# Performance work log

Measured on AMD Instinct MI355X. Metric: run time of the kernel, lower is better.

The kernel has to match this reference:

```python
import jax, jax.numpy as jnp
import numpy as np

B, C, L = 8, 1024, 4096
CTX = 768
NUM_GROUPS = 8
EPS = 1e-5
HEAD_DIM = C  # num_heads = 1 (only shape-consistent config of the module)


def setup_inputs() -> dict:
    key = jax.random.key(0)
    ks = jax.random.split(key, 8)
    s = 0.02
    return {
        "x": jax.random.normal(ks[0], (B, C, L), jnp.float32),
        "context": jax.random.normal(ks[1], (B, CTX), jnp.float32),
        "gn_gamma": jnp.ones((C,), jnp.float32),
        "gn_beta": jnp.zeros((C,), jnp.float32),
        "ln_gamma": jnp.ones((CTX,), jnp.float32),
        "ln_beta": jnp.zeros((CTX,), jnp.float32),
        "Wq": jax.random.normal(ks[2], (C, C), jnp.float32) * s,
        "bq": jnp.zeros((C,), jnp.float32),
        "Wkv": jax.random.normal(ks[3], (2 * C, CTX), jnp.float32) * s,
        "bkv": jnp.zeros((2 * C,), jnp.float32),
        "Wp": jax.random.normal(ks[4], (C, C), jnp.float32) * s,
        "bp": jnp.zeros((C,), jnp.float32),
    }


def group_norm(x, gamma, beta):
    # x: (B, C, L) -> normalize within each of NUM_GROUPS groups over (C//G, L)
    b, c, l = x.shape
    xg = x.reshape(b, NUM_GROUPS, c // NUM_GROUPS, l)
    mu = xg.mean(axis=(2, 3), keepdims=True)
    var = xg.var(axis=(2, 3), keepdims=True)
    xg = (xg - mu) * jax.lax.rsqrt(var + EPS)
    return xg.reshape(b, c, l) * gamma[None, :, None] + beta[None, :, None]


def layer_norm(x, gamma, beta):
    mu = x.mean(axis=-1, keepdims=True)
    var = x.var(axis=-1, keepdims=True)
    return (x - mu) * jax.lax.rsqrt(var + EPS) * gamma + beta


def reference(x, context, gn_gamma, gn_beta, ln_gamma, ln_beta,
              Wq, bq, Wkv, bkv, Wp, bp):
    residual = x
    xn = group_norm(x, gn_gamma, gn_beta)                   # (B, C, L)
    ctx = layer_norm(context, ln_gamma, ln_beta)            # (B, CTX)
    # 1x1 conv Q projection == channel GEMM
    q = jnp.einsum('bcl,oc->bol', xn, Wq) + bq[None, :, None]  # (B, C, L)
    kv = ctx @ Wkv.T + bkv                                  # (B, 2C)
    k, v = kv[:, :C], kv[:, C:]                             # each (B, C) = (B, head_dim)
    scale = HEAD_DIM ** (-0.5)
    # per-position score against the single context key; softmax over L
    attn = jax.nn.softmax(jnp.einsum('bcl,bc->bl', q, k) * scale, axis=-1)  # (B, L)
    # broadcast-weighted outer product (fused form of expand+mul+sum over heads=1)
    out = attn[:, None, :] * v[:, :, None]                  # (B, C, L)
    out = jnp.einsum('bcl,oc->bol', out, Wp) + bp[None, :, None]
    return residual + out
```

## Files before the change

### kernel.cpp

```cpp
#include <hip/hip_runtime.h>
#include <math.h>

#define NB   8
#define NC   1024
#define NL   4096
#define NCTX 768
#define EPSV 1e-5f
#define SCALEV 0.03125f

typedef float floatx4 __attribute__((ext_vector_type(4)));

enum : int {
  OFF_KV    = 0,
  OFF_PV    = 16384,
  OFF_QP    = 24576,
  OFF_SPART = 548864,
  OFF_TPART = 552960,
  OFF_ATTN  = 1077248,
  OFF_S     = 1110016,
  WS_FLOATS = 1110024
};

__device__ __forceinline__ float breduce_sum(float v, float* red) {
  int t = threadIdx.x;
  red[t] = v; __syncthreads();
  for (int s = 128; s > 0; s >>= 1) { if (t < s) red[t] += red[t + s]; __syncthreads(); }
  float r = red[0]; __syncthreads();
  return r;
}
__device__ __forceinline__ float wave_sum(float v) {
  #pragma unroll
  for (int off = 32; off > 0; off >>= 1) v += __shfl_xor(v, off, 64);
  return v;
}

__global__ void k_head(const float* __restrict__ ctx, const float* __restrict__ lng,
                       const float* __restrict__ lnb, const float* __restrict__ Wkv,
                       const float* __restrict__ bkv, const float* __restrict__ Wq,
                       const float* __restrict__ Wp,  float* __restrict__ ws) {
  __shared__ __align__(16) float scf[8 * NCTX];
  __shared__ float sk[8 * 16];
  int t = threadIdx.x, bid = blockIdx.x;
  int wave = t >> 6, lane = t & 63;
  if (bid == 0 && t < NB) ws[OFF_S + t] = 0.f;

  if (bid < 128) {
    #pragma unroll
    for (int bb = 0; bb < 2; bb++) {
      int b = wave * 2 + bb;
      const float* row = ctx + b * NCTX;
      float v[12];
      float s = 0.f;
      #pragma unroll
      for (int k = 0; k < 12; k++) { v[k] = row[lane + 64 * k]; s += v[k]; }
      float mu = wave_sum(s) * (1.0f / NCTX);
      float s2 = 0.f;
      #pragma unroll
      for (int k = 0; k < 12; k++) { float d = v[k] - mu; s2 = fmaf(d, d, s2); }
      float rstd = rsqrtf(wave_sum(s2) * (1.0f / NCTX) + EPSV);
      #pragma unroll
      for (int k = 0; k < 12; k++) {
        int j = lane + 64 * k;
        scf[b * NCTX + j] = (v[k] - mu) * rstd * lng[j] + lnb[j];
      }
    }
    __syncthreads();
    const float4* W4 = reinterpret_cast<const float4*>(Wkv);
    const float4* sc4 = reinterpret_cast<const float4*>(scf);
    #pragma unroll
    for (int rr = 0; rr < 4; rr++) {
      int j = bid * 16 + wave * 4 + rr;
      float4 wv0 = W4[(size_t)j * 192 + lane];
      float4 wv1 = W4[(size_t)j * 192 + lane + 64];
      float4 wv2 = W4[(size_t)j * 192 + lane + 128];
      #pragma unroll
      for (int b = 0; b < 8; b++) {
        const float4* sb = sc4 + b * 192;
        float4 c0 = sb[lane], c1 = sb[lane + 64], c2 = sb[lane + 128];
        float a = wv0.x*c0.x + wv0.y*c0.y + wv0.z*c0.z + wv0.w*c0.w
                + wv1.x*c1.x + wv1.y*c1.y + wv1.z*c1.z + wv1.w*c1.w
                + wv2.x*c2.x + wv2.y*c2.y + wv2.z*c2.z + wv2.w*c2.w;
        a = wave_sum(a);
        if (lane == 0) {
          ws[OFF_KV + b * 2048 + j] = a + bkv[j];
          if (bid < 64) sk[b * 16 + (wave * 4 + rr)] = a + bkv[j];
        }
      }
    }
    if (bid < 64) {
      __syncthreads();
      const float4* Wq4 = reinterpret_cast<const float4*>(Wq);
      float4 acc[8];
      #pragma unroll
      for (int b = 0; b < 8; b++) acc[b] = make_float4(0.f, 0.f, 0.f, 0.f);
      int o0 = bid * 16;
      #pragma unroll 4
      for (int oi = 0; oi < 16; oi++) {
        float4 w = Wq4[(size_t)(o0 + oi) * 256 + t];
        #pragma unroll
        for (int b = 0; b < 8; b++) {
          float kk = sk[b * 16 + oi];
          acc[b].x = fmaf(kk, w.x, acc[b].x);
          acc[b].y = fmaf(kk, w.y, acc[b].y);
          acc[b].z = fmaf(kk, w.z, acc[b].z);
          acc[b].w = fmaf(kk, w.w, acc[b].w);
        }
      }
      float4* qp4 = reinterpret_cast<float4*>(ws + OFF_QP);
      #pragma unroll
      for (int b = 0; b < 8; b++) qp4[(bid * 8 + b) * 256 + t] = acc[b];
    }
  } else {
    const float4* Wp4 = reinterpret_cast<const float4*>(Wp);
    int pid = bid - 128;
    float acc = 0.f;
    for (int idx = pid * 256 + t; idx < 262144; idx += 128 * 256) {
      float4 v = Wp4[idx];
      acc += v.x + v.y + v.z + v.w;
    }
    asm volatile("" :: "v"(acc));
  }
}

__global__ void k_pass1(const float* __restrict__ x, const float* __restrict__ gng,
                        float* __restrict__ ws) {
  __shared__ float red[256];
  __shared__ float sw[64];
  __shared__ __align__(16) float4 part[192];
  int t  = threadIdx.x;
  int lc = blockIdx.x;
  int cs = blockIdx.y;
  int bz = blockIdx.z;
  int b = bz >> 3, g = bz & 7;
  int c0 = g * 128 + cs * 64;
  {
    int cl = t & 63, sp = t >> 6;
    const float* qp = ws + OFF_QP + b * 1024 + c0 + cl;
    float s = 0.f;
    #pragma unroll 4
    for (int oc = sp * 16; oc < sp * 16 + 16; oc++) s += qp[(size_t)oc * 8192];
    red[t] = s;
    __syncthreads();
    if (t < 64) sw[t] = gng[c0 + t] * ((red[t] + red[t + 64]) + (red[t + 128] + red[t + 192]));
    __syncthreads();
  }
  int tl = t & 63, q = t >> 6;
  int l4 = lc * 64 + tl;
  const float4* x4 = reinterpret_cast<const float4*>(x);
  float4 tacc = make_float4(0.f, 0.f, 0.f, 0.f);
  float s1 = 0.f, s2 = 0.f;
  #pragma unroll 4
  for (int ci = q * 16; ci < q * 16 + 16; ci++) {
    float w = sw[ci];
    float4 v = x4[(size_t)(b * NC + c0 + ci) * 1024 + l4];
    tacc.x = fmaf(w, v.x, tacc.x);
    tacc.y = fmaf(w, v.y, tacc.y);
    tacc.z = fmaf(w, v.z, tacc.z);
    tacc.w = fmaf(w, v.w, tacc.w);
    s1 += (v.x + v.y) + (v.z + v.w);
    s2 = fmaf(v.x, v.x, s2); s2 = fmaf(v.y, v.y, s2);
    s2 = fmaf(v.z, v.z, s2); s2 = fmaf(v.w, v.w, s2);
  }
  if (q > 0) part[(q - 1) * 64 + tl] = tacc;
  __syncthreads();
  if (q == 0) {
    float4 p0 = part[tl], p1 = part[64 + tl], p2 = part[128 + tl];
    tacc.x += (p0.x + p1.x) + p2.x;
    tacc.y += (p0.y + p1.y) + p2.y;
    tacc.z += (p0.z + p1.z) + p2.z;
    tacc.w += (p0.w + p1.w) + p2.w;
    reinterpret_cast<float4*>(ws + OFF_TPART)[(size_t)(bz * 2 + cs) * 1024 + l4] = tacc;
  }
  float S1 = breduce_sum(s1, red);
  float S2 = breduce_sum(s2, red);
  if (t == 0) {
    float* sp = ws + OFF_SPART + (bz * 32 + cs * 16 + lc) * 2;
    sp[0] = S1; sp[1] = S2;
  }
}

__global__ void k_tail(const float* __restrict__ Wp, float* __restrict__ ws) {
  __shared__ __align__(16) char smem[32768];
  int t = threadIdx.x, bid = blockIdx.x;
  if (bid < 64) {
    float* srstd = (float*)smem;
    float* red   = (float*)(smem + 1024);
    int lc = bid & 7, b = bid >> 3;
    if (t < 8) {
      const float* sp = ws + OFF_SPART + (b * 8 + t) * 64;
      float S1 = 0.f, S2 = 0.f;
      #pragma unroll
      for (int i = 0; i < 32; i++) { S1 += sp[i * 2]; S2 += sp[i * 2 + 1]; }
      const float invN = 1.0f / (128.0f * (float)NL);
      float mu = S1 * invN;
      float var = S2 * invN - mu * mu;
      srstd[t] = rsqrtf(var + EPSV);
    }
    __syncthreads();
    float esum = 0.f;
    #pragma unroll
    for (int r = 0; r < 2; r++) {
      int l = lc * 512 + r * 256 + t;
      float acc = 0.f;
      #pragma unroll
      for (int g = 0; g < 8; g++) {
        const float* tg = ws + OFF_TPART + (size_t)(b * 8 + g) * 8192;
        acc = fmaf(srstd[g], tg[l] + tg[4096 + l], acc);
      }
      float e = expf(fminf(SCALEV * acc, 60.0f));
      ws[OFF_ATTN + b * NL + l] = e;
      esum += e;
    }
    float tot = breduce_sum(esum, red);
    if (t == 0) atomicAdd(ws + OFF_S + b, tot);
  } else {
    float4* sbuf = (float4*)smem;
    const float4* kv4 = reinterpret_cast<const float4*>(ws + OFF_KV);
    #pragma unroll
    for (int rep = 0; rep < 8; rep++) {
      int idx = rep * 256 + t;
      int b = idx >> 8, i = idx & 255;
      sbuf[idx] = kv4[b * 512 + 256 + i];
    }
    __syncthreads();
    int wave = t >> 6, lane = t & 63;
    const float4* Wp4 = reinterpret_cast<const float4*>(Wp);
    #pragma unroll
    for (int rr = 0; rr < 2; rr++) {
      int o = (bid - 64) * 8 + wave * 2 + rr;
      float4 w0 = Wp4[(size_t)o * 256 + lane];
      float4 w1 = Wp4[(size_t)o * 256 + lane + 64];
      float4 w2 = Wp4[(size_t)o * 256 + lane + 128];
      float4 w3 = Wp4[(size_t)o * 256 + lane + 192];
      #pragma unroll
      for (int b = 0; b < 8; b++) {
        const float4* sb = sbuf + b * 256;
        float4 c0 = sb[lane], c1 = sb[lane + 64], c2 = sb[lane + 128], c3 = sb[lane + 192];
        float a = w0.x*c0.x + w0.y*c0.y + w0.z*c0.z + w0.w*c0.w
                + w1.x*c1.x + w1.y*c1.y + w1.z*c1.z + w1.w*c1.w
                + w2.x*c2.x + w2.y*c2.y + w2.z*c2.z + w2.w*c2.w
                + w3.x*c3.x + w3.y*c3.y + w3.z*c3.z + w3.w*c3.w;
        a = wave_sum(a);
        if (lane == 0) ws[OFF_PV + b * NC + o] = a;
      }
    }
  }
}

__global__ void k_out(const float* __restrict__ x, const float* __restrict__ bp,
                      const float* __restrict__ ws, float* __restrict__ out) {
  const float4* x4 = reinterpret_cast<const float4*>(x);
  floatx4* o4 = reinterpret_cast<floatx4*>(out);
  const float4* a4 = reinterpret_cast<const float4*>(ws + OFF_ATTN);
  const float* pv = ws + OFF_PV;
  const float* Ss = ws + OFF_S;
  const size_t NT4 = (size_t)NB * NC * NL / 4;
  for (size_t i = (size_t)blockIdx.x * blockDim.x + threadIdx.x; i < NT4;
       i += (size_t)gridDim.x * blockDim.x) {
    int b  = (int)(i >> 20);
    int c  = (int)((i >> 10) & (NC - 1));
    int l4 = (int)(i & 1023);
    float4 xv = x4[i];
    float4 av = a4[(size_t)b * 1024 + l4];
    float p  = pv[b * NC + c] / Ss[b];
    float bb = bp[c];
    floatx4 r;
    r.x = xv.x + fmaf(av.x, p, bb);
    r.y = xv.y + fmaf(av.y, p, bb);
    r.z = xv.z + fmaf(av.z, p, bb);
    r.w = xv.w + fmaf(av.w, p, bb);
    __builtin_nontemporal_store(r, &o4[i]);
  }
}

extern "C" void kernel_launch(void* const* d_in, const int* in_sizes, int n_in,
                              void* d_out, int out_size, void* d_ws, size_t ws_size,
                              hipStream_t stream) {
  const float* x    = (const float*)d_in[0];
  const float* ctx  = (const float*)d_in[1];
  const float* gng  = (const float*)d_in[2];
  const float* lng  = (const float*)d_in[4];
  const float* lnb  = (const float*)d_in[5];
  const float* Wq   = (const float*)d_in[6];
  const float* Wkv  = (const float*)d_in[8];
  const float* bkv  = (const float*)d_in[9];
  const float* Wp   = (const float*)d_in[10];
  const float* bp   = (const float*)d_in[11];
  float* ws  = (float*)d_ws;
  float* out = (float*)d_out;

  hipLaunchKernelGGL(k_head,   dim3(256),        dim3(256), 0, stream, ctx, lng, lnb, Wkv, bkv, Wq, Wp, ws);
  hipLaunchKernelGGL(k_pass1,  dim3(16, 2, 64),  dim3(256), 0, stream, x, gng, ws);
  hipLaunchKernelGGL(k_tail,   dim3(192),        dim3(256), 0, stream, Wp, ws);
  hipLaunchKernelGGL(k_out,    dim3(2048),       dim3(256), 0, stream, x, bp, ws, out);
}
```

Measured before the change: 94.93 us.

## Fuse softmax and Wp·v tail into output kernel, widen pass1 channel tiles

Removes the separate k_tail launch. Each output block now recomputes the softmax exponentials for its batch row into shared memory, computes its own four Wp·v dot products, and writes the residual output directly, so the global attn/pv/S buffers and the atomic are gone. pass1 now covers all 128 channels of a group per block rather than two 64-channel halves, which halves the partial writes. The cost is that every one of the 2048 output blocks redoes the 4096-element exp and 8-way partial sum for its batch (256x redundant), and pass1 has half as many blocks.

```diff
diff --git a/kernel.cpp b/kernel.cpp
--- a/kernel.cpp
+++ b/kernel.cpp
@@ -12,13 +12,10 @@
 
 enum : int {
   OFF_KV    = 0,
-  OFF_PV    = 16384,
-  OFF_QP    = 24576,
-  OFF_SPART = 548864,
-  OFF_TPART = 552960,
-  OFF_ATTN  = 1077248,
-  OFF_S     = 1110016,
-  WS_FLOATS = 1110024
+  OFF_QP    = 16384,
+  OFF_SPART = 540672,
+  OFF_TPART = 542720,
+  WS_FLOATS = 804864
 };
 
 __device__ __forceinline__ float breduce_sum(float v, float* red) {
@@ -42,7 +39,6 @@
   __shared__ float sk[8 * 16];
   int t = threadIdx.x, bid = blockIdx.x;
   int wave = t >> 6, lane = t & 63;
-  if (bid == 0 && t < NB) ws[OFF_S + t] = 0.f;
 
   if (bid < 128) {
     #pragma unroll
@@ -125,23 +121,22 @@
 __global__ void k_pass1(const float* __restrict__ x, const float* __restrict__ gng,
                         float* __restrict__ ws) {
   __shared__ float red[256];
-  __shared__ float sw[64];
+  __shared__ float sw[128];
   __shared__ __align__(16) float4 part[192];
   int t  = threadIdx.x;
   int lc = blockIdx.x;
-  int cs = blockIdx.y;
-  int bz = blockIdx.z;
+  int bz = blockIdx.y;
   int b = bz >> 3, g = bz & 7;
-  int c0 = g * 128 + cs * 64;
+  int c0 = g * 128;
   {
-    int cl = t & 63, sp = t >> 6;
+    int cl = t & 127, sp = t >> 7;
     const float* qp = ws + OFF_QP + b * 1024 + c0 + cl;
     float s = 0.f;
     #pragma unroll 4
-    for (int oc = sp * 16; oc < sp * 16 + 16; oc++) s += qp[(size_t)oc * 8192];
+    for (int oc = sp * 32; oc < sp * 32 + 32; oc++) s += qp[(size_t)oc * 8192];
     red[t] = s;
     __syncthreads();
-    if (t < 64) sw[t] = gng[c0 + t] * ((red[t] + red[t + 64]) + (red[t + 128] + red[t + 192]));
+    if (t < 128) sw[t] = gng[c0 + t] * (red[t] + red[t + 128]);
     __syncthreads();
   }
   int tl = t & 63, q = t >> 6;
@@ -150,7 +145,7 @@
   float4 tacc = make_float4(0.f, 0.f, 0.f, 0.f);
   float s1 = 0.f, s2 = 0.f;
   #pragma unroll 4
-  for (int ci = q * 16; ci < q * 16 + 16; ci++) {
+  for (int ci = q * 32; ci < q * 32 + 32; ci++) {
     float w = sw[ci];
     float4 v = x4[(size_t)(b * NC + c0 + ci) * 1024 + l4];
     tacc.x = fmaf(w, v.x, tacc.x);
@@ -169,107 +164,87 @@
     tacc.y += (p0.y + p1.y) + p2.y;
     tacc.z += (p0.z + p1.z) + p2.z;
     tacc.w += (p0.w + p1.w) + p2.w;
-    reinterpret_cast<float4*>(ws + OFF_TPART)[(size_t)(bz * 2 + cs) * 1024 + l4] = tacc;
+    reinterpret_cast<float4*>(ws + OFF_TPART)[(size_t)bz * 1024 + l4] = tacc;
   }
   float S1 = breduce_sum(s1, red);
   float S2 = breduce_sum(s2, red);
   if (t == 0) {
-    float* sp = ws + OFF_SPART + (bz * 32 + cs * 16 + lc) * 2;
+    float* sp = ws + OFF_SPART + (bz * 16 + lc) * 2;
     sp[0] = S1; sp[1] = S2;
   }
 }
 
-__global__ void k_tail(const float* __restrict__ Wp, float* __restrict__ ws) {
-  __shared__ __align__(16) char smem[32768];
+__global__ void k_out(const float* __restrict__ x, const float* __restrict__ bp,
+                      const float* __restrict__ Wp, const float* __restrict__ ws,
+                      float* __restrict__ out) {
+  __shared__ __align__(16) float e_row[NL];
+  __shared__ float red[256];
+  __shared__ float srstd[8];
+  __shared__ float pvv[4];
   int t = threadIdx.x, bid = blockIdx.x;
-  if (bid < 64) {
-    float* srstd = (float*)smem;
-    float* red   = (float*)(smem + 1024);
-    int lc = bid & 7, b = bid >> 3;
-    if (t < 8) {
-      const float* sp = ws + OFF_SPART + (b * 8 + t) * 64;
-      float S1 = 0.f, S2 = 0.f;
-      #pragma unroll
-      for (int i = 0; i < 32; i++) { S1 += sp[i * 2]; S2 += sp[i * 2 + 1]; }
-      const float invN = 1.0f / (128.0f * (float)NL);
-      float mu = S1 * invN;
-      float var = S2 * invN - mu * mu;
-      srstd[t] = rsqrtf(var + EPSV);
-    }
-    __syncthreads();
-    float esum = 0.f;
-    #pragma unroll
-    for (int r = 0; r < 2; r++) {
-      int l = lc * 512 + r * 256 + t;
-      float acc = 0.f;
-      #pragma unroll
-      for (int g = 0; g < 8; g++) {
-        const float* tg = ws + OFF_TPART + (size_t)(b * 8 + g) * 8192;
-        acc = fmaf(srstd[g], tg[l] + tg[4096 + l], acc);
-      }
-      float e = expf(fminf(SCALEV * acc, 60.0f));
-      ws[OFF_ATTN + b * NL + l] = e;
-      esum += e;
-    }
-    float tot = breduce_sum(esum, red);
-    if (t == 0) atomicAdd(ws + OFF_S + b, tot);
-  } else {
-    float4* sbuf = (float4*)smem;
-    const float4* kv4 = reinterpret_cast<const float4*>(ws + OFF_KV);
-    #pragma unroll
-    for (int rep = 0; rep < 8; rep++) {
-      int idx = rep * 256 + t;
-      int b = idx >> 8, i = idx & 255;
-      sbuf[idx] = kv4[b * 512 + 256 + i];
-    }
-    __syncthreads();
-    int wave = t >> 6, lane = t & 63;
+  int b = bid >> 8, chunk = bid & 255;
+  int wave = t >> 6, lane = t & 63;
+
+  {
+    int c = chunk * 4 + wave;
     const float4* Wp4 = reinterpret_cast<const float4*>(Wp);
-    #pragma unroll
-    for (int rr = 0; rr < 2; rr++) {
-      int o = (bid - 64) * 8 + wave * 2 + rr;
-      float4 w0 = Wp4[(size_t)o * 256 + lane];
-      float4 w1 = Wp4[(size_t)o * 256 + lane + 64];
-      float4 w2 = Wp4[(size_t)o * 256 + lane + 128];
-      float4 w3 = Wp4[(size_t)o * 256 + lane + 192];
-      #pragma unroll
-      for (int b = 0; b < 8; b++) {
-        const float4* sb = sbuf + b * 256;
-        float4 c0 = sb[lane], c1 = sb[lane + 64], c2 = sb[lane + 128], c3 = sb[lane + 192];
-        float a = w0.x*c0.x + w0.y*c0.y + w0.z*c0.z + w0.w*c0.w
-                + w1.x*c1.x + w1.y*c1.y + w1.z*c1.z + w1.w*c1.w
-                + w2.x*c2.x + w2.y*c2.y + w2.z*c2.z + w2.w*c2.w
-                + w3.x*c3.x + w3.y*c3.y + w3.z*c3.z + w3.w*c3.w;
-        a = wave_sum(a);
-        if (lane == 0) ws[OFF_PV + b * NC + o] = a;
-      }
-    }
-  }
-}
-
-__global__ void k_out(const float* __restrict__ x, const float* __restrict__ bp,
-                      const float* __restrict__ ws, float* __restrict__ out) {
+    const float4* v4  = reinterpret_cast<const float4*>(ws + OFF_KV) + b * 512 + 256;
+    float s = 0.f;
+    #pragma unroll
+    for (int k = 0; k < 4; k++) {
+      int j = lane + k * 64;
+      float4 wv = Wp4[(size_t)c * 256 + j];
+      float4 vv = v4[j];
+      s += wv.x*vv.x + wv.y*vv.y + wv.z*vv.z + wv.w*vv.w;
+    }
+    s = wave_sum(s);
+    if (lane == 0) pvv[wave] = s;
+  }
+  if (t < 8) {
+    const float* sp = ws + OFF_SPART + (b * 8 + t) * 32;
+    float S1 = 0.f, S2 = 0.f;
+    #pragma unroll
+    for (int i = 0; i < 16; i++) { S1 += sp[i * 2]; S2 += sp[i * 2 + 1]; }
+    const float invN = 1.0f / (128.0f * (float)NL);
+    float mu = S1 * invN;
+    float var = S2 * invN - mu * mu;
+    srstd[t] = rsqrtf(var + EPSV);
+  }
+  __syncthreads();
+  float esum = 0.f;
+  #pragma unroll
+  for (int r = 0; r < 16; r++) {
+    int l = r * 256 + t;
+    float acc = 0.f;
+    #pragma unroll
+    for (int g = 0; g < 8; g++) {
+      const float* tg = ws + OFF_TPART + (size_t)(b * 8 + g) * 4096;
+      acc = fmaf(srstd[g], tg[l], acc);
+    }
+    float e = expf(fminf(SCALEV * acc, 60.0f));
+    e_row[l] = e;
+    esum += e;
+  }
+  float S = breduce_sum(esum, red);
+  float invS = 1.0f / S;
   const float4* x4 = reinterpret_cast<const float4*>(x);
   floatx4* o4 = reinterpret_cast<floatx4*>(out);
-  const float4* a4 = reinterpret_cast<const float4*>(ws + OFF_ATTN);
-  const float* pv = ws + OFF_PV;
-  const float* Ss = ws + OFF_S;
-  const size_t NT4 = (size_t)NB * NC * NL / 4;
-  for (size_t i = (size_t)blockIdx.x * blockDim.x + threadIdx.x; i < NT4;
-       i += (size_t)gridDim.x * blockDim.x) {
-    int b  = (int)(i >> 20);
-    int c  = (int)((i >> 10) & (NC - 1));
-    int l4 = (int)(i & 1023);
-    float4 xv = x4[i];
-    float4 av = a4[(size_t)b * 1024 + l4];
-    float p  = pv[b * NC + c] / Ss[b];
-    float bb = bp[c];
-    floatx4 r;
-    r.x = xv.x + fmaf(av.x, p, bb);
-    r.y = xv.y + fmaf(av.y, p, bb);
-    r.z = xv.z + fmaf(av.z, p, bb);
-    r.w = xv.w + fmaf(av.w, p, bb);
-    __builtin_nontemporal_store(r, &o4[i]);
+  const float4* e4 = reinterpret_cast<const float4*>(e_row);
+  size_t base = (size_t)bid * 4096;
+  #pragma unroll
+  for (int r = 0; r < 16; r++) {
+    int idx = r * 256 + t;
+    int cl = idx >> 10, l4 = idx & 1023;
+    float4 xv = x4[base + idx];
+    float4 ev = e4[l4];
+    float p  = pvv[cl] * invS;
+    float bb = bp[chunk * 4 + cl];
+    floatx4 rr;
+    rr.x = xv.x + fmaf(ev.x, p, bb);
+    rr.y = xv.y + fmaf(ev.y, p, bb);
+    rr.z = xv.z + fmaf(ev.z, p, bb);
+    rr.w = xv.w + fmaf(ev.w, p, bb);
+    __builtin_nontemporal_store(rr, &o4[base + idx]);
   }
 }
 
@@ -289,8 +264,7 @@
   float* ws  = (float*)d_ws;
   float* out = (float*)d_out;
 
-  hipLaunchKernelGGL(k_head,   dim3(256),        dim3(256), 0, stream, ctx, lng, lnb, Wkv, bkv, Wq, Wp, ws);
-  hipLaunchKernelGGL(k_pass1,  dim3(16, 2, 64),  dim3(256), 0, stream, x, gng, ws);
-  hipLaunchKernelGGL(k_tail,   dim3(192),        dim3(256), 0, stream, Wp, ws);
-  hipLaunchKernelGGL(k_out,    dim3(2048),       dim3(256), 0, stream, x, bp, ws, out);
-}
+  hipLaunchKernelGGL(k_head,  dim3(256),      dim3(256), 0, stream, ctx, lng, lnb, Wkv, bkv, Wq, Wp, ws);
+  hipLaunchKernelGGL(k_pass1, dim3(16, 64),   dim3(256), 0, stream, x, gng, ws);
+  hipLaunchKernelGGL(k_out,   dim3(2048),     dim3(256), 0, stream, x, bp, Wp, ws, out);
+}
```

New measurement: 95.97 us. About the same (+1.1%).
